# Optimization experiments

Hardware: AMD Instinct MI355X
Metric: run time of the kernel (lower is better)

## Reference

```python
import jax, jax.numpy as jnp
import numpy as np

N = 8192; E = 262144
CS = 384; CZ = 128; CH = 16; H = 12; PQK = 4; PV = 8
INF = 1e5; EPS = 1e-8
S_QK = float(1.0 / np.sqrt(3.0 * CH))        # sqrt(1/(3*c_hidden))
S_B = float(1.0 / np.sqrt(3.0))              # sqrt(1/3)
S_PT = float(1.0 / np.sqrt(3.0 * (PQK * 9.0 / 2.0)))


def setup_inputs() -> dict:
    key = jax.random.key(0)
    ks = jax.random.split(key, 16)
    def w(k, shape, fan_in):
        return jax.random.normal(k, shape, jnp.float32) * (1.0 / float(np.sqrt(fan_in)))
    d = {}
    d["s"] = jax.random.normal(ks[0], (N, CS), jnp.float32)
    d["z"] = jax.random.normal(ks[1], (E, CZ), jnp.float32)
    d["edge_index"] = jax.random.randint(ks[2], (2, E), 0, N, jnp.int32)
    d["rot"] = jax.random.normal(ks[3], (N, 3, 3), jnp.float32)
    d["trans"] = jax.random.normal(ks[4], (N, 3), jnp.float32)
    d["mask"] = jnp.ones((N,), jnp.float32)
    d["q_w"] = w(ks[5], (CS, H * CH), CS);              d["q_b"] = jnp.zeros((H * CH,), jnp.float32)
    d["kv_w"] = w(ks[6], (CS, 2 * H * CH), CS);         d["kv_b"] = jnp.zeros((2 * H * CH,), jnp.float32)
    d["qp_w"] = w(ks[7], (CS, H * PQK * 3), CS);        d["qp_b"] = jnp.zeros((H * PQK * 3,), jnp.float32)
    d["kvp_w"] = w(ks[8], (CS, H * (PQK + PV) * 3), CS); d["kvp_b"] = jnp.zeros((H * (PQK + PV) * 3,), jnp.float32)
    d["b_w"] = w(ks[9], (CZ, H), CZ);                   d["b_b"] = jnp.zeros((H,), jnp.float32)
    d["dz_w"] = w(ks[10], (CZ, CZ // 4), CZ);           d["dz_b"] = jnp.zeros((CZ // 4,), jnp.float32)
    d["head_weights"] = jnp.full((H,), float(np.log(np.e - 1.0)), jnp.float32)
    cdim = H * (CZ // 4 + CH + PV * 4)
    d["out_w"] = w(ks[11], (cdim, CS), cdim);           d["out_b"] = jnp.zeros((CS,), jnp.float32)
    return d


def reference(s, z, edge_index, rot, trans, mask,
              q_w, q_b, kv_w, kv_b, qp_w, qp_b, kvp_w, kvp_b,
              b_w, b_b, dz_w, dz_b, head_weights, out_w, out_b):
    src = edge_index[1]
    dst = edge_index[0]

    def to_pts(y, P):
        # y: [N, H*P*3] -> split into (x,y,z) chunks -> [N, H*P, 3], then rigid-apply
        xyz = jnp.stack(jnp.split(y, 3, axis=-1), axis=-1)          # [N, H*P, 3]
        pts = jnp.einsum('nij,npj->npi', rot, xyz) + trans[:, None, :]
        return pts.reshape(N, H, P, 3)

    q = (s @ q_w + q_b).reshape(N, H, CH)
    kv = (s @ kv_w + kv_b).reshape(N, H, 2 * CH)
    k, v = kv[..., :CH], kv[..., CH:]

    q_pts = to_pts(s @ qp_w + qp_b, PQK)                            # [N,H,PQK,3]
    kv_pts = to_pts(s @ kvp_w + kvp_b, PQK + PV)                    # [N,H,PQK+PV,3]
    k_pts, v_pts = kv_pts[..., :PQK, :], kv_pts[..., PQK:, :]

    b = z @ b_w + b_b                                               # [E, H]

    # scalar attention logits
    a = jnp.einsum('ehc,ehc->eh', q[src], k[dst]) * S_QK + S_B * b  # [E, H]

    # point attention logits
    disp = q_pts[src] - k_pts[dst]                                  # [E,H,PQK,3]
    pt_att = jnp.sum(disp * disp, axis=-1)                          # [E,H,PQK]
    hw = jax.nn.softplus(head_weights) * S_PT                       # [H]
    pt_att = -0.5 * jnp.sum(pt_att * hw[None, :, None], axis=-1)    # [E,H]

    edge_mask = INF * (mask[dst] * mask[src] - 1.0)                 # [E]
    a = a + pt_att + edge_mask[:, None]

    # scatter softmax over src segments (pyg-style)
    amax = jax.ops.segment_max(a, src, num_segments=N)
    amax = jnp.where(jnp.isfinite(amax), amax, 0.0)
    ex = jnp.exp(a - amax[src])
    denom = jax.ops.segment_sum(ex, src, num_segments=N)
    a = ex / (denom[src] + 1e-16)                                   # [E,H]

    # weighted scatter-reduce aggregations
    o = jax.ops.segment_sum(a[..., None] * v[dst], src, num_segments=N).reshape(N, H * CH)
    o_pt = jax.ops.segment_sum(a[..., None, None] * v_pts[dst], src, num_segments=N)  # [N,H,PV,3]
    # invert_apply: R^T (p - t)
    o_pt = jnp.einsum('nji,nhpj->nhpi', rot, o_pt - trans[:, None, None, :])
    o_pt_norm = jnp.sqrt(jnp.sum(o_pt * o_pt, axis=-1) + EPS).reshape(N, H * PV)
    o_pt_flat = o_pt.reshape(N, H * PV, 3)

    pair_z = z @ dz_w + dz_b                                        # [E, CZ//4]
    o_pair = jax.ops.segment_sum(a[..., None] * pair_z[:, None, :], src, num_segments=N).reshape(N, H * (CZ // 4))

    feats = jnp.concatenate(
        [o, o_pt_flat[..., 0], o_pt_flat[..., 1], o_pt_flat[..., 2], o_pt_norm, o_pair], axis=-1)
    return feats @ out_w + out_b
```

## Files before the change

kernel.cpp:

```cpp
#include <hip/hip_runtime.h>
#include <math.h>

#define NN 8192
#define EE 262144
#define CSD 384
#define CZD 128
#define HH 12
#define MAXDEG 96
#define ABLD 13

#define S_QK 0.14433756729740643f
#define S_B  0.5773502691896258f
#define S_PT 0.1360827634879543f

typedef __bf16 bf16;
typedef __attribute__((ext_vector_type(8))) __bf16 bf16x8;
typedef __attribute__((ext_vector_type(4))) __bf16 bf16x4;
typedef __attribute__((ext_vector_type(4))) float floatx4;

#define OFF_LIN    0
#define OFF_QPACK  (OFF_LIN + NN*1152)
#define OFF_KPACKH (OFF_QPACK + NN*336)
#define OFF_VPACKH (OFF_KPACKH + NN*192)
#define OFF_BLOG   (OFF_VPACKH + NN*240)
#define OFF_PAIRH  (OFF_BLOG + EE*12)
#define OFF_SBF    (OFF_PAIRH + EE*16)
#define OFF_WCAT   (OFF_SBF + NN*192)
#define OFF_OWT    (OFF_WCAT + 221184)
#define OFF_FEATB  (OFF_OWT + 184320)
#define OFF_BZW    (OFF_FEATB + NN*480)
#define OFF_BZB    (OFF_BZW + 3072)
#define OFF_BIASC  (OFF_BZB + 48)
#define OFF_INTS   (OFF_BIASC + 1152)

__global__ void count_kernel(const int* __restrict__ ei, int* __restrict__ counts) {
    int e = blockIdx.x * 256 + threadIdx.x;
    if (e < EE) atomicAdd(&counts[ei[EE + e]], 1);
}

__global__ __launch_bounds__(1024) void scan_kernel(const int* __restrict__ counts,
                                                    int* __restrict__ offs,
                                                    int* __restrict__ cursor) {
    __shared__ int part[1024];
    int t = threadIdx.x;
    int local[8];
    int s = 0;
    #pragma unroll
    for (int j = 0; j < 8; ++j) { local[j] = counts[t * 8 + j]; s += local[j]; }
    part[t] = s;
    __syncthreads();
    for (int off = 1; off < 1024; off <<= 1) {
        int vv = 0;
        if (t >= off) vv = part[t - off];
        __syncthreads();
        if (t >= off) part[t] += vv;
        __syncthreads();
    }
    int run = (t == 0) ? 0 : part[t - 1];
    #pragma unroll
    for (int j = 0; j < 8; ++j) {
        offs[t * 8 + j] = run;
        cursor[t * 8 + j] = run;
        run += local[j];
    }
    if (t == 1023) offs[NN] = run;
}

__global__ void fill_kernel(const int* __restrict__ ei, int* __restrict__ cursor,
                            int* __restrict__ elist) {
    int e = blockIdx.x * 256 + threadIdx.x;
    if (e < EE) {
        int s = ei[EE + e];
        int pos = atomicAdd(&cursor[s], 1);
        elist[pos] = e;
    }
}

__global__ __launch_bounds__(1024) void sort_kernel(const int* __restrict__ offs,
                                                    int* __restrict__ order) {
    __shared__ int hist[256];
    __shared__ int base[256];
    int t = threadIdx.x;
    if (t < 256) hist[t] = 0;
    __syncthreads();
    for (int n = t; n < NN; n += 1024) {
        int d = offs[n + 1] - offs[n];
        if (d > 255) d = 255;
        atomicAdd(&hist[d], 1);
    }
    __syncthreads();
    if (t == 0) {
        int run = 0;
        for (int d = 255; d >= 0; --d) { base[d] = run; run += hist[d]; }
    }
    __syncthreads();
    for (int n = t; n < NN; n += 1024) {
        int d = offs[n + 1] - offs[n];
        if (d > 255) d = 255;
        int pos = atomicAdd(&base[d], 1);
        order[pos] = n;
    }
}

__global__ void cvt_s_kernel(const float* __restrict__ s, bf16* __restrict__ sbf) {
    int i = blockIdx.x * 256 + threadIdx.x;
    float4 v = *(const float4*)(s + (long)i * 4);
    bf16x4 o = {(__bf16)v.x, (__bf16)v.y, (__bf16)v.z, (__bf16)v.w};
    *(bf16x4*)(sbf + (long)i * 4) = o;
}

__global__ void build_wcat(const float* __restrict__ q_w, const float* __restrict__ kv_w,
                           const float* __restrict__ qp_w, const float* __restrict__ kvp_w,
                           const float* __restrict__ q_b, const float* __restrict__ kv_b,
                           const float* __restrict__ qp_b, const float* __restrict__ kvp_b,
                           bf16* __restrict__ wt, float* __restrict__ bias_cat) {
    int id = blockIdx.x * 256 + threadIdx.x;
    if (id >= 1152 * 384) return;
    int n = id / 384, k = id - n * 384;
    float v;
    if (n < 192)      v = q_w[k * 192 + n];
    else if (n < 576) v = kv_w[k * 384 + (n - 192)];
    else if (n < 720) v = qp_w[k * 144 + (n - 576)];
    else              v = kvp_w[k * 432 + (n - 720)];
    wt[id] = (__bf16)v;
    if (k == 0) {
        float b;
        if (n < 192)      b = q_b[n];
        else if (n < 576) b = kv_b[n - 192];
        else if (n < 720) b = qp_b[n - 576];
        else              b = kvp_b[n - 720];
        bias_cat[n] = b;
    }
}

__global__ void build_owt(const float* __restrict__ out_w, bf16* __restrict__ wt) {
    int id = blockIdx.x * 256 + threadIdx.x;
    if (id >= 384 * 960) return;
    int n = id / 960, k = id - n * 960;
    wt[id] = (__bf16)out_w[k * 384 + n];
}

__global__ void build_bzw(const float* __restrict__ b_w, const float* __restrict__ b_b,
                          const float* __restrict__ dz_w, const float* __restrict__ dz_b,
                          bf16* __restrict__ wt, float* __restrict__ bias) {
    int id = blockIdx.x * 256 + threadIdx.x;
    if (id < 48 * 128) {
        int c = id / 128, k = id - c * 128;
        float v = 0.f;
        if (c < 12)      v = b_w[k * 12 + c];
        else if (c < 44) v = dz_w[k * 32 + (c - 12)];
        wt[id] = (__bf16)v;
    }
    if (id < 44) bias[id] = (id < 12) ? b_b[id] : dz_b[id - 12];
}

#define LDKP 40
__global__ __launch_bounds__(256) void gemm_mfma_bt(const bf16* __restrict__ A,
                                                    const bf16* __restrict__ BT,
                                                    const float* __restrict__ bias,
                                                    float* __restrict__ C,
                                                    int M, int K, int N) {
    __shared__ __align__(16) bf16 As[128][LDKP];
    __shared__ __align__(16) bf16 Bs[128][LDKP];
    const int tid = threadIdx.x;
    const int bm = blockIdx.y * 128;
    const int bn = blockIdx.x * 128;
    const int wave = tid >> 6, lane = tid & 63;
    const int wr = (wave >> 1) * 64;
    const int wc = (wave & 1) * 64;
    const int lm = lane & 15;
    const int kg = lane >> 4;

    floatx4 acc[4][4];
    #pragma unroll
    for (int i = 0; i < 4; ++i)
        #pragma unroll
        for (int j = 0; j < 4; ++j) acc[i][j] = (floatx4){0.f, 0.f, 0.f, 0.f};

    const int srow = tid >> 2;
    const int skoff = (tid & 3) * 8;

    for (int k0 = 0; k0 < K; k0 += 32) {
        __syncthreads();
        *(float4*)(&As[srow][skoff])      = *(const float4*)(A + (long)(bm + srow) * K + k0 + skoff);
        *(float4*)(&As[srow + 64][skoff]) = *(const float4*)(A + (long)(bm + srow + 64) * K + k0 + skoff);
        *(float4*)(&Bs[srow][skoff])      = *(const float4*)(BT + (long)(bn + srow) * K + k0 + skoff);
        *(float4*)(&Bs[srow + 64][skoff]) = *(const float4*)(BT + (long)(bn + srow + 64) * K + k0 + skoff);
        __syncthreads();
        bf16x8 af[4], bfr[4];
        #pragma unroll
        for (int i = 0; i < 4; ++i) af[i] = *(const bf16x8*)(&As[wr + i * 16 + lm][kg * 8]);
        #pragma unroll
        for (int j = 0; j < 4; ++j) bfr[j] = *(const bf16x8*)(&Bs[wc + j * 16 + lm][kg * 8]);
        #pragma unroll
        for (int i = 0; i < 4; ++i)
            #pragma unroll
            for (int j = 0; j < 4; ++j)
                acc[i][j] = __builtin_amdgcn_mfma_f32_16x16x32_bf16(af[i], bfr[j], acc[i][j], 0, 0, 0);
    }

    const int crow0 = bm + wr + kg * 4;
    const int ccol0 = bn + wc + lm;
    #pragma unroll
    for (int i = 0; i < 4; ++i) {
        #pragma unroll
        for (int j = 0; j < 4; ++j) {
            int col = ccol0 + j * 16;
            float b = bias[col];
            #pragma unroll
            for (int r = 0; r < 4; ++r)
                C[(long)(crow0 + i * 16 + r) * N + col] = acc[i][j][r] + b;
        }
    }
}

#define BZLD 136
__global__ __launch_bounds__(256) void gemm_bz(const float* __restrict__ z,
                                               const bf16* __restrict__ BT,
                                               const float* __restrict__ bias,
                                               float* __restrict__ blog,
                                               bf16* __restrict__ pairh) {
    __shared__ __align__(16) bf16 Bs[48][BZLD];
    const int tid = threadIdx.x;
    const int bm = blockIdx.x * 128;
    for (int idx = tid; idx < 48 * 16; idx += 256) {
        int r = idx >> 4, seg = idx & 15;
        *(bf16x8*)(&Bs[r][seg * 8]) = *(const bf16x8*)(BT + r * 128 + seg * 8);
    }
    __syncthreads();
    const int wave = tid >> 6, lane = tid & 63;
    const int lm = lane & 15, kg = lane >> 4;
    const int rowbase = wave * 32;
    floatx4 acc[2][3];
    #pragma unroll
    for (int i = 0; i < 2; ++i)
        #pragma unroll
        for (int j = 0; j < 3; ++j) acc[i][j] = (floatx4){0.f, 0.f, 0.f, 0.f};
    #pragma unroll
    for (int ks = 0; ks < 4; ++ks) {
        bf16x8 af[2], bfr[3];
        #pragma unroll
        for (int i = 0; i < 2; ++i) {
            const float* zp = z + (long)(bm + rowbase + i * 16 + lm) * 128 + ks * 32 + kg * 8;
            float4 a0 = *(const float4*)zp;
            float4 a1 = *(const float4*)(zp + 4);
            af[i] = (bf16x8){(__bf16)a0.x, (__bf16)a0.y, (__bf16)a0.z, (__bf16)a0.w,
                             (__bf16)a1.x, (__bf16)a1.y, (__bf16)a1.z, (__bf16)a1.w};
        }
        #pragma unroll
        for (int j = 0; j < 3; ++j) bfr[j] = *(const bf16x8*)(&Bs[j * 16 + lm][ks * 32 + kg * 8]);
        #pragma unroll
        for (int i = 0; i < 2; ++i)
            #pragma unroll
            for (int j = 0; j < 3; ++j)
                acc[i][j] = __builtin_amdgcn_mfma_f32_16x16x32_bf16(af[i], bfr[j], acc[i][j], 0, 0, 0);
    }
    #pragma unroll
    for (int i = 0; i < 2; ++i) {
        int r0 = bm + rowbase + i * 16 + kg * 4;
        #pragma unroll
        for (int j = 0; j < 3; ++j) {
            int col = j * 16 + lm;
            if (col < 12) {
                float b = bias[col];
                #pragma unroll
                for (int r = 0; r < 4; ++r)
                    blog[(long)(r0 + r) * 12 + col] = acc[i][j][r] + b;
            } else if (col < 44) {
                float b = bias[col];
                #pragma unroll
                for (int r = 0; r < 4; ++r)
                    pairh[(long)(r0 + r) * 32 + (col - 12)] = (__bf16)(acc[i][j][r] + b);
            }
        }
    }
}

__global__ void pack_kernel(const float* __restrict__ lin,
                            const float* __restrict__ rot, const float* __restrict__ trans,
                            float* __restrict__ qpack, bf16* __restrict__ kpackh,
                            bf16* __restrict__ vpackh) {
    int n = blockIdx.x;
    int t = threadIdx.x;
    const float* row = lin + (long)n * 1152;
    const float* R = rot + n * 9;
    float tx = trans[n * 3 + 0], ty = trans[n * 3 + 1], tz = trans[n * 3 + 2];
    {
        int h = t >> 4, c = t & 15;
        qpack[(long)n * 336 + h * 28 + c] = row[h * 16 + c];
        kpackh[(long)n * 384 + h * 32 + c] = (__bf16)row[192 + h * 32 + c];
        vpackh[(long)n * 480 + h * 40 + c] = (__bf16)row[192 + h * 32 + 16 + c];
    }
    if (t < 48 && (t & 3) == 0) {
        int h = t >> 2;
        #pragma unroll
        for (int j = 0; j < 4; ++j) kpackh[(long)n * 384 + h * 32 + 28 + j] = (__bf16)0.f;
    }
    float x, y, z;
    if (t < 48) {
        x = row[576 + t]; y = row[624 + t]; z = row[672 + t];
    } else {
        int u = t - 48;
        x = row[720 + u]; y = row[864 + u]; z = row[1008 + u];
    }
    float ox = R[0] * x + R[1] * y + R[2] * z + tx;
    float oy = R[3] * x + R[4] * y + R[5] * z + ty;
    float oz = R[6] * x + R[7] * y + R[8] * z + tz;
    if (t < 48) {
        int h = t >> 2, p = t & 3;
        long b = (long)n * 336 + h * 28 + 16 + p * 3;
        qpack[b] = ox; qpack[b + 1] = oy; qpack[b + 2] = oz;
    } else {
        int u = t - 48;
        int h = u / 12, j = u - h * 12;
        if (j < 4) {
            long b = (long)n * 384 + h * 32 + 16 + j * 3;
            kpackh[b] = (__bf16)ox; kpackh[b + 1] = (__bf16)oy; kpackh[b + 2] = (__bf16)oz;
        } else {
            long b = (long)n * 480 + h * 40 + 16 + (j - 4) * 3;
            vpackh[b] = (__bf16)ox; vpackh[b + 1] = (__bf16)oy; vpackh[b + 2] = (__bf16)oz;
        }
    }
}

__global__ __launch_bounds__(256, 6) void agg_fused(const int* __restrict__ offs,
                                                 const int* __restrict__ elist,
                                                 const int* __restrict__ ei,
                                                 const int* __restrict__ order,
                                                 const float* __restrict__ qpack,
                                                 const bf16* __restrict__ kpackh,
                                                 const bf16* __restrict__ vpackh,
                                                 const float* __restrict__ blog,
                                                 const bf16* __restrict__ pairh,
                                                 const float* __restrict__ mask,
                                                 const float* __restrict__ head_w,
                                                 const float* __restrict__ rot,
                                                 const float* __restrict__ trans,
                                                 bf16* __restrict__ feats) {
    const int wave = threadIdx.x >> 6;
    const int lane = threadIdx.x & 63;
    const int n = order[blockIdx.x * 4 + wave];

    __shared__ float abuf_all[4][MAXDEG * ABLD];
    __shared__ __align__(16) float q_all[4][352];
    __shared__ int smeta_all[4][MAXDEG];
    float* abuf  = abuf_all[wave];
    float* q_s   = q_all[wave];
    int*   smeta = smeta_all[wave];

    const int beg = offs[n];
    int deg = offs[n + 1] - beg;
    if (deg > MAXDEG) deg = MAXDEG;

    for (int idx = lane; idx < 84; idx += 64)
        *(float4*)(&q_s[idx * 4]) = *(const float4*)(qpack + (long)n * 336 + idx * 4);
    if (lane < 12) q_s[336 + lane] = log1pf(expf(head_w[lane])) * S_PT;
    const float msrc = mask[n];

    if (lane < deg) {
        int e = elist[beg + lane];
        int d = ei[e];
        unsigned mb = (mask[d] != 0.f) ? 1u : 0u;
        smeta[lane] = (int)(((unsigned)e << 14) | ((unsigned)d << 1) | mb);
    }
    if (64 + lane < deg) {
        int e = elist[beg + 64 + lane];
        int d = ei[e];
        unsigned mb = (mask[d] != 0.f) ? 1u : 0u;
        smeta[64 + lane] = (int)(((unsigned)e << 14) | ((unsigned)d << 1) | mb);
    }
    __syncthreads();

    for (int idx = lane; idx < deg * 12; idx += 64) {
        int c = idx / 12, h = idx - c * 12;
        const unsigned mm = (unsigned)smeta[c];
        const int e = (int)(mm >> 14);
        const int d = (int)((mm >> 1) & 8191u);
        const float md = (float)(mm & 1u);
        const bf16* khp = kpackh + (long)d * 384 + h * 32;
        bf16x8 k0 = *(const bf16x8*)khp;
        bf16x8 k1 = *(const bf16x8*)(khp + 8);
        bf16x8 p0 = *(const bf16x8*)(khp + 16);
        bf16x8 p1 = *(const bf16x8*)(khp + 24);
        const float* qh = &q_s[h * 28];
        float qk = 0.f, pt = 0.f;
        #pragma unroll
        for (int i = 0; i < 8; ++i) qk += qh[i] * (float)k0[i];
        #pragma unroll
        for (int i = 0; i < 8; ++i) qk += qh[8 + i] * (float)k1[i];
        #pragma unroll
        for (int i = 0; i < 8; ++i) { float dd = qh[16 + i] - (float)p0[i]; pt += dd * dd; }
        #pragma unroll
        for (int i = 0; i < 4; ++i) { float dd = qh[24 + i] - (float)p1[i]; pt += dd * dd; }
        float b = blog[(long)e * 12 + h];
        abuf[c * ABLD + h] = qk * S_QK + S_B * b - 0.5f * q_s[336 + h] * pt
                           + 100000.0f * (msrc * md - 1.0f);
    }
    __syncthreads();

    {
        float lg0[12], lg1[12];
        const bool a0 = lane < deg, a1 = 64 + lane < deg;
        #pragma unroll
        for (int h = 0; h < 12; ++h) {
            lg0[h] = a0 ? abuf[lane * ABLD + h] : -1e30f;
            lg1[h] = a1 ? abuf[(64 + lane) * ABLD + h] : -1e30f;
        }
        #pragma unroll
        for (int h = 0; h < 12; ++h) {
            float mx = fmaxf(lg0[h], lg1[h]);
            #pragma unroll
            for (int off = 32; off > 0; off >>= 1) mx = fmaxf(mx, __shfl_xor(mx, off));
            if (!isfinite(mx)) mx = 0.f;
            float w0 = a0 ? __expf(lg0[h] - mx) : 0.f;
            float w1 = a1 ? __expf(lg1[h] - mx) : 0.f;
            float sm = w0 + w1;
            #pragma unroll
            for (int off = 32; off > 0; off >>= 1) sm += __shfl_xor(sm, off);
            float rl = 1.f / (sm + 1e-16f);
            if (a0) abuf[lane * ABLD + h] = w0 * rl;
            if (a1) abuf[(64 + lane) * ABLD + h] = w1 * rl;
        }
    }
    __syncthreads();

    int hh[2], off8[2];
    bool pr[2], act[2];
    #pragma unroll
    for (int r = 0; r < 2; ++r) {
        int slot = r * 64 + lane;
        if (slot < 60) {
            hh[r] = slot / 5;
            off8[r] = hh[r] * 40 + (slot - hh[r] * 5) * 8;
            pr[r] = false; act[r] = true;
        } else if (slot < 108) {
            int u2 = slot - 60;
            hh[r] = u2 >> 2;
            off8[r] = (u2 & 3) * 8;
            pr[r] = true; act[r] = true;
        } else {
            hh[r] = 0; off8[r] = 0; pr[r] = false; act[r] = false;
        }
    }
    float acc[2][8];
    #pragma unroll
    for (int r = 0; r < 2; ++r)
        #pragma unroll
        for (int i = 0; i < 8; ++i) acc[r][i] = 0.f;

    #pragma unroll 2
    for (int c = 0; c < deg; ++c) {
        const unsigned mm = (unsigned)smeta[c];
        const int eC = (int)(mm >> 14);
        const int dC = (int)((mm >> 1) & 8191u);
        const bf16* vpb = vpackh + (long)dC * 480;
        const bf16* ppb = pairh + (long)eC * 32;
        #pragma unroll
        for (int r = 0; r < 2; ++r) {
            if (act[r]) {
                float w = abuf[c * ABLD + hh[r]];
                bf16x8 v = *(const bf16x8*)((pr[r] ? ppb : vpb) + off8[r]);
                #pragma unroll
                for (int i = 0; i < 8; ++i) acc[r][i] += w * (float)v[i];
            }
        }
    }

    float* opt_s = q_s;
    #pragma unroll
    for (int r = 0; r < 2; ++r) {
        if (!act[r]) continue;
        int slot = r * 64 + lane;
        if (!pr[r]) {
            int h = hh[r], u = slot - h * 5;
            if (u < 2) {
                bf16* fp = feats + (long)n * 960 + h * 16 + u * 8;
                bf16x4 o1 = {(__bf16)acc[r][0], (__bf16)acc[r][1], (__bf16)acc[r][2], (__bf16)acc[r][3]};
                bf16x4 o2 = {(__bf16)acc[r][4], (__bf16)acc[r][5], (__bf16)acc[r][6], (__bf16)acc[r][7]};
                *(bf16x4*)fp = o1;
                *(bf16x4*)(fp + 4) = o2;
            } else {
                float* op = &opt_s[h * 24 + (u - 2) * 8];
                *(floatx4*)op = (floatx4){acc[r][0], acc[r][1], acc[r][2], acc[r][3]};
                *(floatx4*)(op + 4) = (floatx4){acc[r][4], acc[r][5], acc[r][6], acc[r][7]};
            }
        } else {
            int u2 = slot - 60, h = u2 >> 2, seg = u2 & 3;
            bf16* fp = feats + (long)n * 960 + 576 + h * 32 + seg * 8;
            bf16x4 o1 = {(__bf16)acc[r][0], (__bf16)acc[r][1], (__bf16)acc[r][2], (__bf16)acc[r][3]};
            bf16x4 o2 = {(__bf16)acc[r][4], (__bf16)acc[r][5], (__bf16)acc[r][6], (__bf16)acc[r][7]};
            *(bf16x4*)fp = o1;
            *(bf16x4*)(fp + 4) = o2;
        }
    }
    __syncthreads();

    const float* R = rot + n * 9;
    float tx = trans[n * 3 + 0], ty = trans[n * 3 + 1], tz = trans[n * 3 + 2];
    for (int idx = lane; idx < 96; idx += 64) {
        int h = idx >> 3, p = idx & 7;
        float x = opt_s[h * 24 + p * 3 + 0] - tx;
        float y = opt_s[h * 24 + p * 3 + 1] - ty;
        float zc = opt_s[h * 24 + p * 3 + 2] - tz;
        float ox = R[0] * x + R[3] * y + R[6] * zc;
        float oy = R[1] * x + R[4] * y + R[7] * zc;
        float oz = R[2] * x + R[5] * y + R[8] * zc;
        float nrm = sqrtf(ox * ox + oy * oy + oz * oz + 1e-8f);
        feats[(long)n * 960 + 192 + idx] = (__bf16)ox;
        feats[(long)n * 960 + 288 + idx] = (__bf16)oy;
        feats[(long)n * 960 + 384 + idx] = (__bf16)oz;
        feats[(long)n * 960 + 480 + idx] = (__bf16)nrm;
    }
}

extern "C" void kernel_launch(void* const* d_in, const int* in_sizes, int n_in,
                              void* d_out, int out_size, void* d_ws, size_t ws_size,
                              hipStream_t stream) {
    const float* s      = (const float*)d_in[0];
    const float* z      = (const float*)d_in[1];
    const int*   ei     = (const int*)d_in[2];
    const float* rot    = (const float*)d_in[3];
    const float* trans  = (const float*)d_in[4];
    const float* mask   = (const float*)d_in[5];
    const float* q_w    = (const float*)d_in[6];
    const float* q_b    = (const float*)d_in[7];
    const float* kv_w   = (const float*)d_in[8];
    const float* kv_b   = (const float*)d_in[9];
    const float* qp_w   = (const float*)d_in[10];
    const float* qp_b   = (const float*)d_in[11];
    const float* kvp_w  = (const float*)d_in[12];
    const float* kvp_b  = (const float*)d_in[13];
    const float* b_w    = (const float*)d_in[14];
    const float* b_b    = (const float*)d_in[15];
    const float* dz_w   = (const float*)d_in[16];
    const float* dz_b   = (const float*)d_in[17];
    const float* head_w = (const float*)d_in[18];
    const float* out_w  = (const float*)d_in[19];
    const float* out_b  = (const float*)d_in[20];

    float* ws      = (float*)d_ws;
    float* lin     = ws + OFF_LIN;
    float* qpack   = ws + OFF_QPACK;
    bf16*  kpackh  = (bf16*)(ws + OFF_KPACKH);
    bf16*  vpackh  = (bf16*)(ws + OFF_VPACKH);
    float* blog    = ws + OFF_BLOG;
    bf16*  pairh   = (bf16*)(ws + OFF_PAIRH);
    bf16*  sbf     = (bf16*)(ws + OFF_SBF);
    bf16*  wcat    = (bf16*)(ws + OFF_WCAT);
    bf16*  owt     = (bf16*)(ws + OFF_OWT);
    bf16*  featb   = (bf16*)(ws + OFF_FEATB);
    bf16*  bzwbf   = (bf16*)(ws + OFF_BZW);
    float* bzb     = ws + OFF_BZB;
    float* biasc   = ws + OFF_BIASC;
    int* ints   = (int*)(ws + OFF_INTS);
    int* offs   = ints;
    int* cursor = ints + NN + 1;
    int* counts = ints + 2 * NN + 1;
    int* elist  = ints + 3 * NN + 1;
    int* order  = ints + 3 * NN + 1 + EE;

    hipMemsetAsync(counts, 0, NN * sizeof(int), stream);
    count_kernel<<<EE / 256, 256, 0, stream>>>(ei, counts);
    scan_kernel<<<1, 1024, 0, stream>>>(counts, offs, cursor);
    fill_kernel<<<EE / 256, 256, 0, stream>>>(ei, cursor, elist);
    sort_kernel<<<1, 1024, 0, stream>>>(offs, order);

    cvt_s_kernel<<<NN * CSD / 4 / 256, 256, 0, stream>>>(s, sbf);
    build_wcat<<<(1152 * 384 + 255) / 256, 256, 0, stream>>>(q_w, kv_w, qp_w, kvp_w,
                                                             q_b, kv_b, qp_b, kvp_b, wcat, biasc);
    build_owt<<<(384 * 960 + 255) / 256, 256, 0, stream>>>(out_w, owt);
    build_bzw<<<(48 * 128 + 255) / 256, 256, 0, stream>>>(b_w, b_b, dz_w, dz_b, bzwbf, bzb);

    gemm_mfma_bt<<<dim3(1152 / 128, NN / 128), 256, 0, stream>>>(sbf, wcat, biasc, lin, NN, CSD, 1152);

    pack_kernel<<<NN, 192, 0, stream>>>(lin, rot, trans, qpack, kpackh, vpackh);

    gemm_bz<<<EE / 128, 256, 0, stream>>>(z, bzwbf, bzb, blog, pairh);

    agg_fused<<<NN / 4, 256, 0, stream>>>(offs, elist, ei, order, qpack, kpackh, vpackh,
                                          blog, pairh, mask, head_w, rot, trans, featb);

    gemm_mfma_bt<<<dim3(384 / 128, NN / 128), 256, 0, stream>>>(featb, owt, out_b, (float*)d_out, NN, 960, 384);
}
```

Before: 470.3 us.

## Software-pipeline aggregation gathers, shrink agg blocks, add narrower output GEMM tile

The aggregation loop is rewritten so each lane handles one value slot plus a second pair slot, with a three-deep register prefetch of gathered rows to hide global-load latency. Blocks are halved to two waves each, which reduces shared memory per block and gives finer scheduling granularity. The final output projection uses a new 128x64 tile GEMM, doubling the number of blocks for the N=384 GEMM to fill more CUs. The trade-off is higher register pressure from the prefetch buffers and more blocks to launch.

```diff
diff --git a/kernel.cpp b/kernel.cpp
--- a/kernel.cpp
+++ b/kernel.cpp
@@ -214,6 +214,64 @@
     }
 }
 
+__global__ __launch_bounds__(256) void gemm_mfma_bt_n64(const bf16* __restrict__ A,
+                                                        const bf16* __restrict__ BT,
+                                                        const float* __restrict__ bias,
+                                                        float* __restrict__ C,
+                                                        int M, int K, int N) {
+    __shared__ __align__(16) bf16 As[128][LDKP];
+    __shared__ __align__(16) bf16 Bs[64][LDKP];
+    const int tid = threadIdx.x;
+    const int bm = blockIdx.y * 128;
+    const int bn = blockIdx.x * 64;
+    const int wave = tid >> 6, lane = tid & 63;
+    const int wr = (wave >> 1) * 64;
+    const int wc = (wave & 1) * 32;
+    const int lm = lane & 15;
+    const int kg = lane >> 4;
+
+    floatx4 acc[4][2];
+    #pragma unroll
+    for (int i = 0; i < 4; ++i)
+        #pragma unroll
+        for (int j = 0; j < 2; ++j) acc[i][j] = (floatx4){0.f, 0.f, 0.f, 0.f};
+
+    const int srow = tid >> 2;
+    const int skoff = (tid & 3) * 8;
+
+    for (int k0 = 0; k0 < K; k0 += 32) {
+        __syncthreads();
+        *(float4*)(&As[srow][skoff])      = *(const float4*)(A + (long)(bm + srow) * K + k0 + skoff);
+        *(float4*)(&As[srow + 64][skoff]) = *(const float4*)(A + (long)(bm + srow + 64) * K + k0 + skoff);
+        *(float4*)(&Bs[srow][skoff])      = *(const float4*)(BT + (long)(bn + srow) * K + k0 + skoff);
+        __syncthreads();
+        bf16x8 af[4], bfr[2];
+        #pragma unroll
+        for (int i = 0; i < 4; ++i) af[i] = *(const bf16x8*)(&As[wr + i * 16 + lm][kg * 8]);
+        #pragma unroll
+        for (int j = 0; j < 2; ++j) bfr[j] = *(const bf16x8*)(&Bs[wc + j * 16 + lm][kg * 8]);
+        #pragma unroll
+        for (int i = 0; i < 4; ++i)
+            #pragma unroll
+            for (int j = 0; j < 2; ++j)
+                acc[i][j] = __builtin_amdgcn_mfma_f32_16x16x32_bf16(af[i], bfr[j], acc[i][j], 0, 0, 0);
+    }
+
+    const int crow0 = bm + wr + kg * 4;
+    const int ccol0 = bn + wc + lm;
+    #pragma unroll
+    for (int i = 0; i < 4; ++i) {
+        #pragma unroll
+        for (int j = 0; j < 2; ++j) {
+            int col = ccol0 + j * 16;
+            float b = bias[col];
+            #pragma unroll
+            for (int r = 0; r < 4; ++r)
+                C[(long)(crow0 + i * 16 + r) * N + col] = acc[i][j][r] + b;
+        }
+    }
+}
+
 #define BZLD 136
 __global__ __launch_bounds__(256) void gemm_bz(const float* __restrict__ z,
                                                const bf16* __restrict__ BT,
@@ -323,7 +381,7 @@
     }
 }
 
-__global__ __launch_bounds__(256, 6) void agg_fused(const int* __restrict__ offs,
+__global__ __launch_bounds__(128, 6) void agg_fused(const int* __restrict__ offs,
                                                  const int* __restrict__ elist,
                                                  const int* __restrict__ ei,
                                                  const int* __restrict__ order,
@@ -339,11 +397,11 @@
                                                  bf16* __restrict__ feats) {
     const int wave = threadIdx.x >> 6;
     const int lane = threadIdx.x & 63;
-    const int n = order[blockIdx.x * 4 + wave];
-
-    __shared__ float abuf_all[4][MAXDEG * ABLD];
-    __shared__ __align__(16) float q_all[4][352];
-    __shared__ int smeta_all[4][MAXDEG];
+    const int n = order[blockIdx.x * 2 + wave];
+
+    __shared__ float abuf_all[2][MAXDEG * ABLD];
+    __shared__ __align__(16) float q_all[2][352];
+    __shared__ int smeta_all[2][MAXDEG];
     float* abuf  = abuf_all[wave];
     float* q_s   = q_all[wave];
     int*   smeta = smeta_all[wave];
@@ -424,74 +482,88 @@
     }
     __syncthreads();
 
-    int hh[2], off8[2];
-    bool pr[2], act[2];
-    #pragma unroll
-    for (int r = 0; r < 2; ++r) {
-        int slot = r * 64 + lane;
-        if (slot < 60) {
-            hh[r] = slot / 5;
-            off8[r] = hh[r] * 40 + (slot - hh[r] * 5) * 8;
-            pr[r] = false; act[r] = true;
-        } else if (slot < 108) {
-            int u2 = slot - 60;
-            hh[r] = u2 >> 2;
-            off8[r] = (u2 & 3) * 8;
-            pr[r] = true; act[r] = true;
-        } else {
-            hh[r] = 0; off8[r] = 0; pr[r] = false; act[r] = false;
-        }
-    }
-    float acc[2][8];
-    #pragma unroll
-    for (int r = 0; r < 2; ++r)
-        #pragma unroll
-        for (int i = 0; i < 8; ++i) acc[r][i] = 0.f;
-
-    #pragma unroll 2
-    for (int c = 0; c < deg; ++c) {
-        const unsigned mm = (unsigned)smeta[c];
-        const int eC = (int)(mm >> 14);
-        const int dC = (int)((mm >> 1) & 8191u);
-        const bf16* vpb = vpackh + (long)dC * 480;
-        const bf16* ppb = pairh + (long)eC * 32;
-        #pragma unroll
-        for (int r = 0; r < 2; ++r) {
-            if (act[r]) {
-                float w = abuf[c * ABLD + hh[r]];
-                bf16x8 v = *(const bf16x8*)((pr[r] ? ppb : vpb) + off8[r]);
-                #pragma unroll
-                for (int i = 0; i < 8; ++i) acc[r][i] += w * (float)v[i];
-            }
-        }
-    }
+    int hh0, off80;
+    bool pr0;
+    {
+        int slot = lane;
+        if (slot < 60) { hh0 = slot / 5; off80 = hh0 * 40 + (slot - hh0 * 5) * 8; pr0 = false; }
+        else           { hh0 = 0; off80 = (slot - 60) * 8; pr0 = true; }
+    }
+    const bool a1v = lane < 44;
+    const int hh1 = (lane + 4) >> 2;
+    const int off81 = (lane & 3) * 8;
+
+    float acc0[8], acc1[8];
+    #pragma unroll
+    for (int i = 0; i < 8; ++i) { acc0[i] = 0.f; acc1[i] = 0.f; }
+
+    bf16x8 sA0, sA1, sB0, sB1, sC0, sC1;
+
+#define LOADE(cc, s0, s1) do { \
+        unsigned mmq = (unsigned)smeta[cc]; \
+        const bf16* vpb = vpackh + (long)((mmq >> 1) & 8191u) * 480; \
+        const bf16* ppb = pairh + (long)(mmq >> 14) * 32; \
+        s0 = *(const bf16x8*)((pr0 ? ppb : vpb) + off80); \
+        if (a1v) s1 = *(const bf16x8*)(ppb + off81); \
+    } while (0)
+
+#define ACCUME(cc, s0, s1) do { \
+        float w0 = abuf[(cc) * ABLD + hh0]; \
+        _Pragma("unroll") for (int i = 0; i < 8; ++i) acc0[i] += w0 * (float)s0[i]; \
+        if (a1v) { \
+            float w1 = abuf[(cc) * ABLD + hh1]; \
+            _Pragma("unroll") for (int i = 0; i < 8; ++i) acc1[i] += w1 * (float)s1[i]; \
+        } \
+    } while (0)
+
+    if (deg > 0) LOADE(0, sA0, sA1);
+    if (deg > 1) LOADE(1, sB0, sB1);
+    if (deg > 2) LOADE(2, sC0, sC1);
+    int c = 0;
+    for (; c + 3 <= deg; c += 3) {
+        ACCUME(c, sA0, sA1);
+        if (c + 3 < deg) LOADE(c + 3, sA0, sA1);
+        ACCUME(c + 1, sB0, sB1);
+        if (c + 4 < deg) LOADE(c + 4, sB0, sB1);
+        ACCUME(c + 2, sC0, sC1);
+        if (c + 5 < deg) LOADE(c + 5, sC0, sC1);
+    }
+    if (c < deg)     ACCUME(c, sA0, sA1);
+    if (c + 1 < deg) ACCUME(c + 1, sB0, sB1);
+#undef LOADE
+#undef ACCUME
 
     float* opt_s = q_s;
-    #pragma unroll
-    for (int r = 0; r < 2; ++r) {
-        if (!act[r]) continue;
-        int slot = r * 64 + lane;
-        if (!pr[r]) {
-            int h = hh[r], u = slot - h * 5;
+    {
+        int slot = lane;
+        if (!pr0) {
+            int h = hh0, u = slot - h * 5;
             if (u < 2) {
                 bf16* fp = feats + (long)n * 960 + h * 16 + u * 8;
-                bf16x4 o1 = {(__bf16)acc[r][0], (__bf16)acc[r][1], (__bf16)acc[r][2], (__bf16)acc[r][3]};
-                bf16x4 o2 = {(__bf16)acc[r][4], (__bf16)acc[r][5], (__bf16)acc[r][6], (__bf16)acc[r][7]};
+                bf16x4 o1 = {(__bf16)acc0[0], (__bf16)acc0[1], (__bf16)acc0[2], (__bf16)acc0[3]};
+                bf16x4 o2 = {(__bf16)acc0[4], (__bf16)acc0[5], (__bf16)acc0[6], (__bf16)acc0[7]};
                 *(bf16x4*)fp = o1;
                 *(bf16x4*)(fp + 4) = o2;
             } else {
                 float* op = &opt_s[h * 24 + (u - 2) * 8];
-                *(floatx4*)op = (floatx4){acc[r][0], acc[r][1], acc[r][2], acc[r][3]};
-                *(floatx4*)(op + 4) = (floatx4){acc[r][4], acc[r][5], acc[r][6], acc[r][7]};
+                *(floatx4*)op = (floatx4){acc0[0], acc0[1], acc0[2], acc0[3]};
+                *(floatx4*)(op + 4) = (floatx4){acc0[4], acc0[5], acc0[6], acc0[7]};
             }
         } else {
-            int u2 = slot - 60, h = u2 >> 2, seg = u2 & 3;
-            bf16* fp = feats + (long)n * 960 + 576 + h * 32 + seg * 8;
-            bf16x4 o1 = {(__bf16)acc[r][0], (__bf16)acc[r][1], (__bf16)acc[r][2], (__bf16)acc[r][3]};
-            bf16x4 o2 = {(__bf16)acc[r][4], (__bf16)acc[r][5], (__bf16)acc[r][6], (__bf16)acc[r][7]};
+            int seg = slot - 60;
+            bf16* fp = feats + (long)n * 960 + 576 + seg * 8;
+            bf16x4 o1 = {(__bf16)acc0[0], (__bf16)acc0[1], (__bf16)acc0[2], (__bf16)acc0[3]};
+            bf16x4 o2 = {(__bf16)acc0[4], (__bf16)acc0[5], (__bf16)acc0[6], (__bf16)acc0[7]};
             *(bf16x4*)fp = o1;
             *(bf16x4*)(fp + 4) = o2;
         }
+    }
+    if (a1v) {
+        bf16* fp = feats + (long)n * 960 + 576 + hh1 * 32 + (lane & 3) * 8;
+        bf16x4 o1 = {(__bf16)acc1[0], (__bf16)acc1[1], (__bf16)acc1[2], (__bf16)acc1[3]};
+        bf16x4 o2 = {(__bf16)acc1[4], (__bf16)acc1[5], (__bf16)acc1[6], (__bf16)acc1[7]};
+        *(bf16x4*)fp = o1;
+        *(bf16x4*)(fp + 4) = o2;
     }
     __syncthreads();
 
@@ -577,8 +649,8 @@
 
     gemm_bz<<<EE / 128, 256, 0, stream>>>(z, bzwbf, bzb, blog, pairh);
 
-    agg_fused<<<NN / 4, 256, 0, stream>>>(offs, elist, ei, order, qpack, kpackh, vpackh,
+    agg_fused<<<NN / 2, 128, 0, stream>>>(offs, elist, ei, order, qpack, kpackh, vpackh,
                                           blog, pairh, mask, head_w, rot, trans, featb);
 
-    gemm_mfma_bt<<<dim3(384 / 128, NN / 128), 256, 0, stream>>>(featb, owt, out_b, (float*)d_out, NN, 960, 384);
-}
+    gemm_mfma_bt_n64<<<dim3(384 / 64, NN / 128), 256, 0, stream>>>(featb, owt, out_b, (float*)d_out, NN, 960, 384);
+}
```

Result: slower. 482.9 us (+2.7%).
